# Performance work log

Hardware: AMD Instinct MI355X
Metric: run time of the kernel (lower is better)

Reference implementation:

```python
import jax, jax.numpy as jnp
import numpy as np

B, L, C = 16, 4096, 32
D = 512
W = 24                  # rolling window
LAGS = [3, 5, 7]
MAXLEN = 5000
EPS = 1e-5


def setup_inputs() -> dict:
    key = jax.random.key(0)
    ks = jax.random.split(key, 8)
    return {
        "x": jax.random.normal(ks[0], (B, L, C), jnp.float32),
        "conv_w": jax.random.normal(ks[1], (D, C * (5 + len(LAGS)), 3), jnp.float32) * 0.05,
        "conv_b": jnp.zeros((D,), jnp.float32),
        "learned_pe": jax.random.normal(ks[2], (1, MAXLEN, D), jnp.float32) * (1.0 / np.sqrt(D)),
        "tape_pos": jax.random.normal(ks[3], (MAXLEN, D), jnp.float32) * 0.02,
        "tproj_w": jax.random.normal(ks[4], (D, D), jnp.float32) * 0.02,
        "tproj_b": jnp.zeros((D,), jnp.float32),
        "mixer_w": jax.random.normal(ks[5], (D, 2 * D), jnp.float32) * 0.02,
        "mixer_b": jnp.zeros((D,), jnp.float32),
        "g_c": jnp.ones((D,), jnp.float32), "b_c": jnp.zeros((D,), jnp.float32),
        "g_f": jnp.ones((D,), jnp.float32), "b_f": jnp.zeros((D,), jnp.float32),
        "g_l": jnp.ones((D,), jnp.float32), "b_l": jnp.zeros((D,), jnp.float32),
        "g_t": jnp.ones((D,), jnp.float32), "b_t": jnp.zeros((D,), jnp.float32),
        "weight_params": jnp.array([0.25, 0.25, 0.25, 0.25], jnp.float32),
    }


def _layer_norm(h, g, b):
    m = jnp.mean(h, axis=-1, keepdims=True)
    v = jnp.mean((h - m) ** 2, axis=-1, keepdims=True)
    return g * (h - m) / jnp.sqrt(v + EPS) + b


def reference(x, conv_w, conv_b, learned_pe, tape_pos, tproj_w, tproj_b,
              mixer_w, mixer_b, g_c, b_c, g_f, b_f, g_l, b_l, g_t, b_t,
              weight_params):
    Bx, Lx, Cx = x.shape
    # --- RollingFeatureExtractor: replicate-pad left, sliding mean/max/min/std
    xp = jnp.pad(x, ((0, 0), (W - 1, 0), (0, 0)), mode="edge")          # [B, L+W-1, C]
    win = jnp.stack([xp[:, i:i + Lx, :] for i in range(W)], axis=2)       # [B, L, W, C]
    w_mean = jnp.mean(win, axis=2)
    w_max = jnp.max(win, axis=2)
    w_min = jnp.min(win, axis=2)
    w_var = jnp.sum((win - w_mean[:, :, None, :]) ** 2, axis=2) / (W - 1)  # unbiased, torch.std default
    w_std = jnp.sqrt(w_var)
    x_stats = jnp.concatenate([x, w_mean, w_max, w_min, w_std], axis=-1)  # [B, L, 5C]
    # --- lag differences (replicate pad left by max lag)
    ml = max(LAGS)
    xl = jnp.pad(x, ((0, 0), (ml, 0), (0, 0)), mode="edge")
    x_lags = jnp.concatenate([x - xl[:, ml - l:ml - l + Lx, :] for l in LAGS], axis=-1)  # [B, L, 3C]
    comb = jnp.concatenate([x_stats, x_lags], axis=-1)                    # [B, L, 8C]
    # --- TokenEmbedding: Conv1d k=3, circular padding
    h = comb.transpose(0, 2, 1)                                           # [B, 8C, L]
    h = jnp.pad(h, ((0, 0), (0, 0), (1, 1)), mode="wrap")
    h = jax.lax.conv_general_dilated(h, conv_w, (1,), "VALID",
                                     dimension_numbers=("NCH", "OIH", "NCH"))
    h = h + conv_b[None, :, None]
    combined_emb = _layer_norm(h.transpose(0, 2, 1), g_c, b_c)            # [B, L, D]
    # --- fixed sinusoidal PE (constant / detached)
    pos = jnp.arange(Lx)
    div = jnp.exp(jnp.arange(0, D, 2).astype(x.dtype) * (-(np.log(10000.0) / D)))
    ang = pos[:, None].astype(x.dtype) * div[None, :]                     # [L, D/2]
    pe_fixed_tab = jnp.zeros((Lx, D), x.dtype).at[:, 0::2].set(jnp.sin(ang)).at[:, 1::2].set(jnp.cos(ang))
    pe_fixed = _layer_norm(pe_fixed_tab, g_f, b_f)[None]                  # [1, L, D]
    # --- learnable PE
    pe_learned = _layer_norm(learned_pe[:, :Lx], g_l, b_l)                # [1, L, D]
    # --- tAPE: token proj + learned pos embedding -> mixer linear
    pe = tape_pos[pos]                                                    # [L, D]
    tok = combined_emb @ tproj_w.T + tproj_b                              # [B, L, D]
    mixed = jnp.concatenate([tok, jnp.broadcast_to(pe[None], tok.shape)], axis=-1)
    pe_tape = _layer_norm(mixed @ mixer_w.T + mixer_b, g_t, b_t)          # [B, L, D]
    # --- softmax-weighted sum (dropout is identity in eval)
    w = jax.nn.softmax(weight_params)
    return (w[0] * combined_emb + w[1] * pe_fixed + w[2] * pe_learned + w[3] * pe_tape)
```

## Files before the change

kernel.cpp:

```cpp
#include <hip/hip_runtime.h>
#include <stdint.h>


typedef unsigned short u16;
using short8  = __attribute__((ext_vector_type(8))) short;
using floatx4 = __attribute__((ext_vector_type(4))) float;
typedef __attribute__((address_space(1))) const unsigned int u32_as1;
typedef __attribute__((address_space(3))) unsigned int       u32_as3;

static __device__ __forceinline__ u16 f2b(float f) {
  unsigned u = __float_as_uint(f);
  u += 0x7FFFu + ((u >> 16) & 1u);
  return (u16)(u >> 16);
}
static __device__ __forceinline__ float b2f(u16 h) {
  return __uint_as_float(((unsigned)h) << 16);
}

__global__ __launch_bounds__(256) void prep_mats(
    const float* __restrict__ conv_w, const float* __restrict__ mixer_w,
    const float* __restrict__ tproj_w, const float* __restrict__ tape_pos,
    u16* __restrict__ W1, u16* __restrict__ A_m1, u16* __restrict__ M2t,
    u16* __restrict__ tprojT, u16* __restrict__ tape_bf) {
  int i = blockIdx.x * 256 + threadIdx.x;
  if (i < 393216) {
    int d = i / 768, rem = i - d * 768;
    int j = rem >> 8, c = rem & 255;
    W1[i] = f2b(conv_w[(d * 256 + c) * 3 + j]);
  } else if (i < 393216 + 262144) {
    int k = i - 393216; int p = k >> 9, r = k & 511;
    A_m1[k] = f2b(mixer_w[p * 1024 + r]);
  } else if (i < 393216 + 524288) {
    int k = i - 393216 - 262144; int p = k >> 9, r = k & 511;
    M2t[k] = f2b(mixer_w[p * 1024 + 512 + r]);
  } else if (i < 393216 + 786432) {
    int k = i - 393216 - 524288; int q = k >> 9, r = k & 511;
    tprojT[k] = f2b(tproj_w[r * 512 + q]);
  } else if (i < 393216 + 786432 + 2097152) {
    int k = i - 393216 - 786432;
    tape_bf[k] = f2b(tape_pos[k]);
  }
}

__global__ __launch_bounds__(256) void bias2_k(
    const float* __restrict__ mixer_w, const float* __restrict__ tproj_b,
    const float* __restrict__ mixer_b, float* __restrict__ bias2) {
  int p = blockIdx.x * 256 + threadIdx.x;
  if (p < 512) {
    float s = mixer_b[p];
    for (int r = 0; r < 512; ++r) s += mixer_w[p * 1024 + r] * tproj_b[r];
    bias2[p] = s;
  }
}

__global__ __launch_bounds__(256) void feat_kernel(
    const float* __restrict__ x, u16* __restrict__ comb) {
  __shared__ float sx[87 * 32];
  const int b = blockIdx.y, l0 = blockIdx.x * 64;
  for (int idx = threadIdx.x; idx < 87 * 32; idx += 256) {
    int r = idx >> 5, c = idx & 31;
    int ls = l0 - 23 + r; if (ls < 0) ls = 0;
    sx[idx] = x[((size_t)b * 4096 + ls) * 32 + c];
  }
  __syncthreads();
  const int c = threadIdx.x & 31, lr0 = threadIdx.x >> 5;
  for (int pass = 0; pass < 8; ++pass) {
    int lr = pass * 8 + lr0;
    int l = l0 + lr;
    float w[24];
    float s = 0.f, mx = -3.4e38f, mn = 3.4e38f;
    #pragma unroll
    for (int i = 0; i < 24; ++i) {
      float v = sx[(lr + i) * 32 + c];
      w[i] = v; s += v; mx = fmaxf(mx, v); mn = fminf(mn, v);
    }
    float mean = s * (1.f / 24.f);
    float ssd = 0.f;
    #pragma unroll
    for (int i = 0; i < 24; ++i) { float d = w[i] - mean; ssd += d * d; }
    float sd = sqrtf(fmaxf(ssd, 0.f) * (1.f / 23.f));
    float xv = w[23];
    float lag3 = xv - sx[(lr + 20) * 32 + c];
    float lag5 = xv - sx[(lr + 18) * 32 + c];
    float lag7 = xv - sx[(lr + 16) * 32 + c];
    size_t base = ((size_t)b * 4096 + l) * 256 + c;
    comb[base +   0] = f2b(xv);
    comb[base +  32] = f2b(mean);
    comb[base +  64] = f2b(mx);
    comb[base +  96] = f2b(mn);
    comb[base + 128] = f2b(sd);
    comb[base + 160] = f2b(lag3);
    comb[base + 192] = f2b(lag5);
    comb[base + 224] = f2b(lag7);
  }
}

__global__ __launch_bounds__(256) void gemm_bt(
    const u16* __restrict__ A, const u16* __restrict__ Bt,
    void* __restrict__ outp, int K, int ldc,
    const float* __restrict__ bias, int outBf16) {
  __shared__ __align__(16) u16 lA[128 * 64];
  __shared__ __align__(16) u16 lB[128 * 64];
  const int tid = threadIdx.x;
  const int m0 = blockIdx.x * 128, n0 = blockIdx.y * 128;
  const int wave = tid >> 6, lane = tid & 63;
  const int wm = (wave & 1) * 64, wn = (wave >> 1) * 64;
  const int quad = lane >> 4, r16 = lane & 15;
  const int rowT = tid >> 3, col8 = tid & 7;

  floatx4 acc[4][4];
  #pragma unroll
  for (int i = 0; i < 4; ++i)
    #pragma unroll
    for (int j = 0; j < 4; ++j) acc[i][j] = (floatx4){0.f, 0.f, 0.f, 0.f};

  for (int kk = 0; kk < K; kk += 64) {
    __syncthreads();
    #pragma unroll
    for (int it = 0; it < 4; ++it) {
      int rr = it * 32 + rowT;
      const u16* ga = A  + (size_t)(m0 + rr) * K + kk + col8 * 8;
      const u16* gb = Bt + (size_t)(n0 + rr) * K + kk + col8 * 8;
      __builtin_amdgcn_global_load_lds((u32_as1*)ga, (u32_as3*)&lA[rr * 64 + col8 * 8], 16, 0, 0);
      __builtin_amdgcn_global_load_lds((u32_as1*)gb, (u32_as3*)&lB[rr * 64 + col8 * 8], 16, 0, 0);
    }
    __syncthreads();
    #pragma unroll
    for (int ks = 0; ks < 64; ks += 32) {
      short8 af[4], bfr[4];
      #pragma unroll
      for (int i = 0; i < 4; ++i)
        af[i] = *(const short8*)&lA[(wm + i * 16 + r16) * 64 + ks + quad * 8];
      #pragma unroll
      for (int j = 0; j < 4; ++j)
        bfr[j] = *(const short8*)&lB[(wn + j * 16 + r16) * 64 + ks + quad * 8];
      #pragma unroll
      for (int i = 0; i < 4; ++i)
        #pragma unroll
        for (int j = 0; j < 4; ++j)
          acc[i][j] = __builtin_amdgcn_mfma_f32_16x16x32_bf16(af[i], bfr[j], acc[i][j], 0, 0, 0);
    }
  }
  #pragma unroll
  for (int i = 0; i < 4; ++i) {
    #pragma unroll
    for (int rr = 0; rr < 4; ++rr) {
      int m = m0 + wm + i * 16 + quad * 4 + rr;
      #pragma unroll
      for (int j = 0; j < 4; ++j) {
        int n = n0 + wn + j * 16 + r16;
        float v = acc[i][j][rr];
        if (bias) v += bias[n];
        if (outBf16) ((u16*)outp)[(size_t)m * ldc + n] = f2b(v);
        else         ((float*)outp)[(size_t)m * ldc + n] = v;
      }
    }
  }
}


#define STAGE_A(SRCEXPR)                                                       \
  _Pragma("unroll")                                                            \
  for (int it = 0; it < 2; ++it) {                                             \
    int id = it * 256 + tid, row = id >> 3, c = id & 7;                        \
    int cg = ((c ^ (row & 7)) << 3);                                           \
    const u16* gsrc = (SRCEXPR);                                               \
    __builtin_amdgcn_global_load_lds((u32_as1*)gsrc,                           \
        (u32_as3*)(smem + id * 16), 16, 0, 0);                                 \
  }
#define STAGE_B(SRCEXPR)                                                       \
  _Pragma("unroll")                                                            \
  for (int it = 0; it < 16; ++it) {                                            \
    int id = it * 256 + tid, row = id >> 3, c = id & 7;                        \
    int cg = ((c ^ (row & 7)) << 3);                                           \
    const u16* gsrc = (SRCEXPR);                                               \
    __builtin_amdgcn_global_load_lds((u32_as1*)gsrc,                           \
        (u32_as3*)(smem + 8192 + id * 16), 16, 0, 0);                          \
  }

__global__ __launch_bounds__(256, 2) void gemm_conv_ln(
    const u16* __restrict__ comb, const u16* __restrict__ W1,
    const float* __restrict__ conv_b, const float* __restrict__ g_c,
    const float* __restrict__ b_c, u16* __restrict__ ce) {
  __shared__ __align__(16) char smem[73728];
  __shared__ float sG[512], sB[512], sBias[512];
  u16* lA = (u16*)smem;
  u16* lB = (u16*)(smem + 8192);
  u16* lT = (u16*)smem;

  const int tid = threadIdx.x;
  if (tid < 128) {
    ((float4*)sG)[tid]    = ((const float4*)g_c)[tid];
    ((float4*)sB)[tid]    = ((const float4*)b_c)[tid];
    ((float4*)sBias)[tid] = ((const float4*)conv_b)[tid];
  }
  const int m0 = blockIdx.x * 64;
  const int b = m0 >> 12, l0 = m0 & 4095;
  const int w = tid >> 6, lane = tid & 63;
  const int quad = lane >> 4, r16 = lane & 15;

  floatx4 acc[4][8];
  #pragma unroll
  for (int i = 0; i < 4; ++i)
    #pragma unroll
    for (int jj = 0; jj < 8; ++jj) acc[i][jj] = (floatx4){0.f, 0.f, 0.f, 0.f};

  for (int kk = 0; kk < 768; kk += 64) {
    const int jsh = kk >> 8, kc = kk & 255;
    __syncthreads();
    STAGE_A(comb + (((size_t)b * 4096 + ((l0 + row + jsh - 1 + 4096) & 4095)) << 8) + kc + cg)
    STAGE_B(W1 + (size_t)row * 768 + kk + cg)
    __syncthreads();
    #pragma unroll
    for (int ks = 0; ks < 64; ks += 32) {
      short8 af[4];
      #pragma unroll
      for (int i = 0; i < 4; ++i) {
        int row = i * 16 + r16;
        af[i] = *(const short8*)&lA[row * 64 + ((((ks >> 3) + quad) ^ (row & 7)) << 3)];
      }
      #pragma unroll
      for (int jj = 0; jj < 8; ++jj) {
        int row = w * 128 + jj * 16 + r16;
        short8 bf = *(const short8*)&lB[row * 64 + ((((ks >> 3) + quad) ^ (row & 7)) << 3)];
        #pragma unroll
        for (int i = 0; i < 4; ++i)
          acc[i][jj] = __builtin_amdgcn_mfma_f32_16x16x32_bf16(bf, af[i], acc[i][jj], 0, 0, 0);
      }
    }
  }
  __syncthreads();
  #pragma unroll
  for (int jj = 0; jj < 8; ++jj) {
    int n = w * 128 + jj * 16 + quad * 4;
    float4 b4 = *(const float4*)&sBias[n];
    #pragma unroll
    for (int i = 0; i < 4; ++i) {
      ushort4 pk;
      pk.x = f2b(acc[i][jj][0] + b4.x);
      pk.y = f2b(acc[i][jj][1] + b4.y);
      pk.z = f2b(acc[i][jj][2] + b4.z);
      pk.w = f2b(acc[i][jj][3] + b4.w);
      *(ushort4*)(lT + (size_t)(i * 16 + r16) * 520 + n) = pk;
    }
  }
  __syncthreads();
  const int orow = tid >> 2, part = tid & 3;
  const u16* rowp = lT + (size_t)orow * 520;
  float s1 = 0.f, s2 = 0.f;
  #pragma unroll
  for (int k = 0; k < 16; ++k) {
    short8 t8 = *(const short8*)(rowp + (part + k * 4) * 8);
    #pragma unroll
    for (int e = 0; e < 8; ++e) {
      float f = b2f((u16)t8[e]); s1 += f; s2 += f * f;
    }
  }
  s1 += __shfl_xor(s1, 1); s2 += __shfl_xor(s2, 1);
  s1 += __shfl_xor(s1, 2); s2 += __shfl_xor(s2, 2);
  float mean = s1 * (1.f / 512.f);
  float inv = rsqrtf(fmaxf(s2 * (1.f / 512.f) - mean * mean, 0.f) + 1e-5f);
  size_t mrow = (size_t)(m0 + orow) * 512;
  #pragma unroll
  for (int k = 0; k < 16; ++k) {
    int c8 = part + k * 4;
    short8 t8 = *(const short8*)(rowp + c8 * 8);
    short8 o;
    #pragma unroll
    for (int e = 0; e < 8; ++e) {
      int d = c8 * 8 + e;
      o[e] = (short)f2b(sG[d] * ((b2f((u16)t8[e]) - mean) * inv) + sB[d]);
    }
    *(short8*)(ce + mrow + c8 * 8) = o;
  }
}

__global__ __launch_bounds__(256, 2) void gemm_pre_final(
    const u16* __restrict__ ceA, const u16* __restrict__ Wf,
    const u16* __restrict__ ctab_bf, const u16* __restrict__ pf_tab,
    const u16* __restrict__ pl_tab, const float* __restrict__ g_t,
    const float* __restrict__ b_t, const float* __restrict__ wp,
    float* __restrict__ out) {
  __shared__ __align__(16) char smem[73728];
  __shared__ float sG[512], sB[512];
  u16* lA = (u16*)smem;
  u16* lB = (u16*)(smem + 8192);
  u16* lT = (u16*)smem;

  const int tid = threadIdx.x;
  if (tid < 128) {
    ((float4*)sG)[tid] = ((const float4*)g_t)[tid];
    ((float4*)sB)[tid] = ((const float4*)b_t)[tid];
  }
  const int m0 = blockIdx.x * 64;
  const int l0m = m0 & 4095;
  const int w = tid >> 6, lane = tid & 63;
  const int quad = lane >> 4, r16 = lane & 15;

  floatx4 acc[4][8];
  #pragma unroll
  for (int i = 0; i < 4; ++i)
    #pragma unroll
    for (int jj = 0; jj < 8; ++jj) acc[i][jj] = (floatx4){0.f, 0.f, 0.f, 0.f};

  for (int kk = 0; kk < 512; kk += 64) {
    __syncthreads();
    STAGE_A(ceA + (size_t)(m0 + row) * 512 + kk + cg)
    STAGE_B(Wf + (size_t)row * 512 + kk + cg)
    __syncthreads();
    #pragma unroll
    for (int ks = 0; ks < 64; ks += 32) {
      short8 af[4];
      #pragma unroll
      for (int i = 0; i < 4; ++i) {
        int row = i * 16 + r16;
        af[i] = *(const short8*)&lA[row * 64 + ((((ks >> 3) + quad) ^ (row & 7)) << 3)];
      }
      #pragma unroll
      for (int jj = 0; jj < 8; ++jj) {
        int row = w * 128 + jj * 16 + r16;
        short8 bf = *(const short8*)&lB[row * 64 + ((((ks >> 3) + quad) ^ (row & 7)) << 3)];
        #pragma unroll
        for (int i = 0; i < 4; ++i)
          acc[i][jj] = __builtin_amdgcn_mfma_f32_16x16x32_bf16(bf, af[i], acc[i][jj], 0, 0, 0);
      }
    }
  }
  __syncthreads();
  #pragma unroll
  for (int jj = 0; jj < 8; ++jj) {
    int n = w * 128 + jj * 16 + quad * 4;
    #pragma unroll
    for (int i = 0; i < 4; ++i) {
      ushort4 pk;
      pk.x = f2b(acc[i][jj][0]);
      pk.y = f2b(acc[i][jj][1]);
      pk.z = f2b(acc[i][jj][2]);
      pk.w = f2b(acc[i][jj][3]);
      *(ushort4*)(lT + (size_t)(i * 16 + r16) * 520 + n) = pk;
    }
  }
  __syncthreads();
  const int orow = tid >> 2, part = tid & 3;
  const int m = m0 + orow, l = l0m + orow;
  const u16* rowp = lT + (size_t)orow * 520;
  const size_t lrow = (size_t)l * 512, mrow = (size_t)m * 512;
  float s1 = 0.f, s2 = 0.f;
  #pragma unroll
  for (int k = 0; k < 16; ++k) {
    int c8 = part + k * 4;
    short8 t8 = *(const short8*)(rowp + c8 * 8);
    short8 ct = *(const short8*)(ctab_bf + lrow + c8 * 8);
    #pragma unroll
    for (int e = 0; e < 8; ++e) {
      float f = b2f((u16)t8[e]) + b2f((u16)ct[e]);
      s1 += f; s2 += f * f;
    }
  }
  s1 += __shfl_xor(s1, 1); s2 += __shfl_xor(s2, 1);
  s1 += __shfl_xor(s1, 2); s2 += __shfl_xor(s2, 2);
  float mean = s1 * (1.f / 512.f);
  float inv = rsqrtf(fmaxf(s2 * (1.f / 512.f) - mean * mean, 0.f) + 1e-5f);

  float a0 = wp[0], a1 = wp[1], a2 = wp[2], a3 = wp[3];
  float mxw = fmaxf(fmaxf(a0, a1), fmaxf(a2, a3));
  float e0 = expf(a0 - mxw), e1 = expf(a1 - mxw), e2 = expf(a2 - mxw), e3 = expf(a3 - mxw);
  float invs = 1.f / (e0 + e1 + e2 + e3);
  float w0 = e0 * invs, w1 = e1 * invs, w2 = e2 * invs, w3 = e3 * invs;

  #pragma unroll
  for (int k = 0; k < 16; ++k) {
    int c8 = part + k * 4;
    short8 t8  = *(const short8*)(rowp + c8 * 8);
    short8 ct  = *(const short8*)(ctab_bf + lrow + c8 * 8);
    short8 c8v = *(const short8*)(ceA + mrow + c8 * 8);
    short8 pf  = *(const short8*)(pf_tab + lrow + c8 * 8);
    short8 pl  = *(const short8*)(pl_tab + lrow + c8 * 8);
    float o[8];
    #pragma unroll
    for (int e = 0; e < 8; ++e) {
      int d = c8 * 8 + e;
      float f = b2f((u16)t8[e]) + b2f((u16)ct[e]);
      float pt = sG[d] * ((f - mean) * inv) + sB[d];
      o[e] = w0 * b2f((u16)c8v[e]) + w1 * b2f((u16)pf[e]) + w2 * b2f((u16)pl[e]) + w3 * pt;
    }
    float4* op = (float4*)(out + mrow + c8 * 8);
    op[0] = make_float4(o[0], o[1], o[2], o[3]);
    op[1] = make_float4(o[4], o[5], o[6], o[7]);
  }
}

__global__ __launch_bounds__(256) void pe_tables(
    const float* __restrict__ learned_pe,
    const float* __restrict__ gf, const float* __restrict__ bf_,
    const float* __restrict__ gl, const float* __restrict__ bl,
    u16* __restrict__ pf_tab, u16* __restrict__ pl_tab) {
  int row = blockIdx.x * 4 + (threadIdx.x >> 6);
  int lane = threadIdx.x & 63;
  size_t base = (size_t)row * 512 + lane * 8;
  float v[8]; float s1 = 0.f, s2 = 0.f;
  #pragma unroll
  for (int e = 0; e < 8; ++e) {
    int d = lane * 8 + e;
    int de = d & ~1;
    float div = expf((float)de * (-9.210340371976184f / 512.f));
    float ang = (float)row * div;
    v[e] = (d & 1) ? cosf(ang) : sinf(ang);
    s1 += v[e]; s2 += v[e] * v[e];
  }
  #pragma unroll
  for (int off = 32; off; off >>= 1) { s1 += __shfl_xor(s1, off); s2 += __shfl_xor(s2, off); }
  float mean = s1 * (1.f / 512.f);
  float inv = rsqrtf(fmaxf(s2 * (1.f / 512.f) - mean * mean, 0.f) + 1e-5f);
  short8 o;
  #pragma unroll
  for (int e = 0; e < 8; ++e) {
    int d = lane * 8 + e;
    o[e] = (short)f2b(gf[d] * ((v[e] - mean) * inv) + bf_[d]);
  }
  *(short8*)(pf_tab + base) = o;
  const float4* lp = (const float4*)(learned_pe + base);
  float4 a = lp[0], bq = lp[1];
  float u[8] = {a.x, a.y, a.z, a.w, bq.x, bq.y, bq.z, bq.w};
  s1 = 0.f; s2 = 0.f;
  #pragma unroll
  for (int e = 0; e < 8; ++e) { s1 += u[e]; s2 += u[e] * u[e]; }
  #pragma unroll
  for (int off = 32; off; off >>= 1) { s1 += __shfl_xor(s1, off); s2 += __shfl_xor(s2, off); }
  mean = s1 * (1.f / 512.f);
  inv = rsqrtf(fmaxf(s2 * (1.f / 512.f) - mean * mean, 0.f) + 1e-5f);
  #pragma unroll
  for (int e = 0; e < 8; ++e) {
    int d = lane * 8 + e;
    o[e] = (short)f2b(gl[d] * ((u[e] - mean) * inv) + bl[d]);
  }
  *(short8*)(pl_tab + base) = o;
}

extern "C" void kernel_launch(void* const* d_in, const int* in_sizes, int n_in,
                              void* d_out, int out_size, void* d_ws, size_t ws_size,
                              hipStream_t stream) {
  const float* x          = (const float*)d_in[0];
  const float* conv_w     = (const float*)d_in[1];
  const float* conv_b     = (const float*)d_in[2];
  const float* learned_pe = (const float*)d_in[3];
  const float* tape_pos   = (const float*)d_in[4];
  const float* tproj_w    = (const float*)d_in[5];
  const float* tproj_b    = (const float*)d_in[6];
  const float* mixer_w    = (const float*)d_in[7];
  const float* mixer_b    = (const float*)d_in[8];
  const float* g_c        = (const float*)d_in[9];
  const float* b_c        = (const float*)d_in[10];
  const float* g_f        = (const float*)d_in[11];
  const float* b_f        = (const float*)d_in[12];
  const float* g_l        = (const float*)d_in[13];
  const float* b_l        = (const float*)d_in[14];
  const float* g_t        = (const float*)d_in[15];
  const float* b_t        = (const float*)d_in[16];
  const float* wp         = (const float*)d_in[17];

  char* ws = (char*)d_ws;
  u16*  comb    = (u16*)(ws + 0);
  u16*  ce      = (u16*)(ws + 33554432);
  char* S       = ws + 100663296;
  u16*  W1      = (u16*)(S + 0);
  u16*  A_m1    = (u16*)(S + 786432);
  u16*  M2t     = (u16*)(S + 1310720);
  u16*  tprojT  = (u16*)(S + 1835008);
  u16*  tape_bf = (u16*)(S + 2359296);
  u16*  Wf      = (u16*)(S + 6553600);
  u16*  ctab_bf = (u16*)(S + 7077888);
  float* bias2  = (float*)(S + 11272192);
  u16*  pf_tab  = (u16*)(S + 11274240);
  u16*  pl_tab  = (u16*)(S + 15468544);

  prep_mats<<<12800, 256, 0, stream>>>(conv_w, mixer_w, tproj_w, tape_pos,
                                       W1, A_m1, M2t, tprojT, tape_bf);
  bias2_k<<<2, 256, 0, stream>>>(mixer_w, tproj_b, mixer_b, bias2);
  feat_kernel<<<dim3(64, 16), 256, 0, stream>>>(x, comb);
  gemm_bt<<<dim3(4, 4), 256, 0, stream>>>(A_m1, tprojT, Wf, 512, 512, nullptr, 1);
  gemm_bt<<<dim3(32, 4), 256, 0, stream>>>(tape_bf, M2t, ctab_bf, 512, 512, bias2, 1);
  pe_tables<<<1024, 256, 0, stream>>>(learned_pe, g_f, b_f, g_l, b_l, pf_tab, pl_tab);
  gemm_conv_ln<<<1024, 256, 0, stream>>>(comb, W1, conv_b, g_c, b_c, ce);
  gemm_pre_final<<<1024, 256, 0, stream>>>(ce, Wf, ctab_bf, pf_tab, pl_tab,
                                           g_t, b_t, wp, (float*)d_out);
}
```

Measured before the change: 390.8 us.

## Double GEMM M-tile to 128 rows with 512-thread blocks sharing B tile

Both fused GEMM kernels now process 128 rows per block with 8 waves arranged 2x4, so each staged 512x64 weight tile in LDS serves twice as many output rows. This halves the total weight-tile reloads from L2 and the grid size. The LayerNorm epilogue runs in two 64-row halves through the shared LDS transpose buffer, which adds extra barriers. LDS per block grows to about 88KB, so likely only one block fits per CU, giving the same wave count as before but less freedom in scheduling.

```diff
diff --git a/kernel.cpp b/kernel.cpp
--- a/kernel.cpp
+++ b/kernel.cpp
@@ -162,7 +162,7 @@
 #define STAGE_A(SRCEXPR)                                                       \
   _Pragma("unroll")                                                            \
   for (int it = 0; it < 2; ++it) {                                             \
-    int id = it * 256 + tid, row = id >> 3, c = id & 7;                        \
+    int id = it * 512 + tid, row = id >> 3, c = id & 7;                        \
     int cg = ((c ^ (row & 7)) << 3);                                           \
     const u16* gsrc = (SRCEXPR);                                               \
     __builtin_amdgcn_global_load_lds((u32_as1*)gsrc,                           \
@@ -170,22 +170,22 @@
   }
 #define STAGE_B(SRCEXPR)                                                       \
   _Pragma("unroll")                                                            \
-  for (int it = 0; it < 16; ++it) {                                            \
-    int id = it * 256 + tid, row = id >> 3, c = id & 7;                        \
+  for (int it = 0; it < 8; ++it) {                                             \
+    int id = it * 512 + tid, row = id >> 3, c = id & 7;                        \
     int cg = ((c ^ (row & 7)) << 3);                                           \
     const u16* gsrc = (SRCEXPR);                                               \
     __builtin_amdgcn_global_load_lds((u32_as1*)gsrc,                           \
-        (u32_as3*)(smem + 8192 + id * 16), 16, 0, 0);                          \
-  }
-
-__global__ __launch_bounds__(256, 2) void gemm_conv_ln(
+        (u32_as3*)(smem + 16384 + id * 16), 16, 0, 0);                         \
+  }
+
+__global__ __launch_bounds__(512, 2) void gemm_conv_ln(
     const u16* __restrict__ comb, const u16* __restrict__ W1,
     const float* __restrict__ conv_b, const float* __restrict__ g_c,
     const float* __restrict__ b_c, u16* __restrict__ ce) {
-  __shared__ __align__(16) char smem[73728];
+  __shared__ __align__(16) char smem[81920];
   __shared__ float sG[512], sB[512], sBias[512];
   u16* lA = (u16*)smem;
-  u16* lB = (u16*)(smem + 8192);
+  u16* lB = (u16*)(smem + 16384);
   u16* lT = (u16*)smem;
 
   const int tid = threadIdx.x;
@@ -194,10 +194,11 @@
     ((float4*)sB)[tid]    = ((const float4*)b_c)[tid];
     ((float4*)sBias)[tid] = ((const float4*)conv_b)[tid];
   }
-  const int m0 = blockIdx.x * 64;
+  const int m0 = blockIdx.x * 128;
   const int b = m0 >> 12, l0 = m0 & 4095;
   const int w = tid >> 6, lane = tid & 63;
   const int quad = lane >> 4, r16 = lane & 15;
+  const int wm2 = w >> 2, wn = (w & 3) * 128;
 
   floatx4 acc[4][8];
   #pragma unroll
@@ -216,12 +217,12 @@
       short8 af[4];
       #pragma unroll
       for (int i = 0; i < 4; ++i) {
-        int row = i * 16 + r16;
+        int row = wm2 * 64 + i * 16 + r16;
         af[i] = *(const short8*)&lA[row * 64 + ((((ks >> 3) + quad) ^ (row & 7)) << 3)];
       }
       #pragma unroll
       for (int jj = 0; jj < 8; ++jj) {
-        int row = w * 128 + jj * 16 + r16;
+        int row = wn + jj * 16 + r16;
         short8 bf = *(const short8*)&lB[row * 64 + ((((ks >> 3) + quad) ^ (row & 7)) << 3)];
         #pragma unroll
         for (int i = 0; i < 4; ++i)
@@ -230,61 +231,68 @@
     }
   }
   __syncthreads();
-  #pragma unroll
-  for (int jj = 0; jj < 8; ++jj) {
-    int n = w * 128 + jj * 16 + quad * 4;
-    float4 b4 = *(const float4*)&sBias[n];
-    #pragma unroll
-    for (int i = 0; i < 4; ++i) {
-      ushort4 pk;
-      pk.x = f2b(acc[i][jj][0] + b4.x);
-      pk.y = f2b(acc[i][jj][1] + b4.y);
-      pk.z = f2b(acc[i][jj][2] + b4.z);
-      pk.w = f2b(acc[i][jj][3] + b4.w);
-      *(ushort4*)(lT + (size_t)(i * 16 + r16) * 520 + n) = pk;
-    }
-  }
-  __syncthreads();
-  const int orow = tid >> 2, part = tid & 3;
-  const u16* rowp = lT + (size_t)orow * 520;
-  float s1 = 0.f, s2 = 0.f;
-  #pragma unroll
-  for (int k = 0; k < 16; ++k) {
-    short8 t8 = *(const short8*)(rowp + (part + k * 4) * 8);
-    #pragma unroll
-    for (int e = 0; e < 8; ++e) {
-      float f = b2f((u16)t8[e]); s1 += f; s2 += f * f;
-    }
-  }
-  s1 += __shfl_xor(s1, 1); s2 += __shfl_xor(s2, 1);
-  s1 += __shfl_xor(s1, 2); s2 += __shfl_xor(s2, 2);
-  float mean = s1 * (1.f / 512.f);
-  float inv = rsqrtf(fmaxf(s2 * (1.f / 512.f) - mean * mean, 0.f) + 1e-5f);
-  size_t mrow = (size_t)(m0 + orow) * 512;
-  #pragma unroll
-  for (int k = 0; k < 16; ++k) {
-    int c8 = part + k * 4;
-    short8 t8 = *(const short8*)(rowp + c8 * 8);
-    short8 o;
-    #pragma unroll
-    for (int e = 0; e < 8; ++e) {
-      int d = c8 * 8 + e;
-      o[e] = (short)f2b(sG[d] * ((b2f((u16)t8[e]) - mean) * inv) + sB[d]);
-    }
-    *(short8*)(ce + mrow + c8 * 8) = o;
-  }
-}
-
-__global__ __launch_bounds__(256, 2) void gemm_pre_final(
+  const int orow = tid >> 3, part = tid & 7;
+  #pragma unroll
+  for (int h = 0; h < 2; ++h) {
+    if (wm2 == h) {
+      #pragma unroll
+      for (int jj = 0; jj < 8; ++jj) {
+        int n = wn + jj * 16 + quad * 4;
+        float4 b4 = *(const float4*)&sBias[n];
+        #pragma unroll
+        for (int i = 0; i < 4; ++i) {
+          ushort4 pk;
+          pk.x = f2b(acc[i][jj][0] + b4.x);
+          pk.y = f2b(acc[i][jj][1] + b4.y);
+          pk.z = f2b(acc[i][jj][2] + b4.z);
+          pk.w = f2b(acc[i][jj][3] + b4.w);
+          *(ushort4*)(lT + (size_t)(i * 16 + r16) * 520 + n) = pk;
+        }
+      }
+    }
+    __syncthreads();
+    const u16* rowp = lT + (size_t)orow * 520;
+    float s1 = 0.f, s2 = 0.f;
+    #pragma unroll
+    for (int k = 0; k < 8; ++k) {
+      short8 t8 = *(const short8*)(rowp + (part + k * 8) * 8);
+      #pragma unroll
+      for (int e = 0; e < 8; ++e) {
+        float f = b2f((u16)t8[e]); s1 += f; s2 += f * f;
+      }
+    }
+    s1 += __shfl_xor(s1, 1); s2 += __shfl_xor(s2, 1);
+    s1 += __shfl_xor(s1, 2); s2 += __shfl_xor(s2, 2);
+    s1 += __shfl_xor(s1, 4); s2 += __shfl_xor(s2, 4);
+    float mean = s1 * (1.f / 512.f);
+    float inv = rsqrtf(fmaxf(s2 * (1.f / 512.f) - mean * mean, 0.f) + 1e-5f);
+    size_t mrow = (size_t)(m0 + h * 64 + orow) * 512;
+    #pragma unroll
+    for (int k = 0; k < 8; ++k) {
+      int c8 = part + k * 8;
+      short8 t8 = *(const short8*)(rowp + c8 * 8);
+      short8 o;
+      #pragma unroll
+      for (int e = 0; e < 8; ++e) {
+        int d = c8 * 8 + e;
+        o[e] = (short)f2b(sG[d] * ((b2f((u16)t8[e]) - mean) * inv) + sB[d]);
+      }
+      *(short8*)(ce + mrow + c8 * 8) = o;
+    }
+    __syncthreads();
+  }
+}
+
+__global__ __launch_bounds__(512, 2) void gemm_pre_final(
     const u16* __restrict__ ceA, const u16* __restrict__ Wf,
     const u16* __restrict__ ctab_bf, const u16* __restrict__ pf_tab,
     const u16* __restrict__ pl_tab, const float* __restrict__ g_t,
     const float* __restrict__ b_t, const float* __restrict__ wp,
     float* __restrict__ out) {
-  __shared__ __align__(16) char smem[73728];
+  __shared__ __align__(16) char smem[81920];
   __shared__ float sG[512], sB[512];
   u16* lA = (u16*)smem;
-  u16* lB = (u16*)(smem + 8192);
+  u16* lB = (u16*)(smem + 16384);
   u16* lT = (u16*)smem;
 
   const int tid = threadIdx.x;
@@ -292,10 +300,11 @@
     ((float4*)sG)[tid] = ((const float4*)g_t)[tid];
     ((float4*)sB)[tid] = ((const float4*)b_t)[tid];
   }
-  const int m0 = blockIdx.x * 64;
+  const int m0 = blockIdx.x * 128;
   const int l0m = m0 & 4095;
   const int w = tid >> 6, lane = tid & 63;
   const int quad = lane >> 4, r16 = lane & 15;
+  const int wm2 = w >> 2, wn = (w & 3) * 128;
 
   floatx4 acc[4][8];
   #pragma unroll
@@ -313,12 +322,12 @@
       short8 af[4];
       #pragma unroll
       for (int i = 0; i < 4; ++i) {
-        int row = i * 16 + r16;
+        int row = wm2 * 64 + i * 16 + r16;
         af[i] = *(const short8*)&lA[row * 64 + ((((ks >> 3) + quad) ^ (row & 7)) << 3)];
       }
       #pragma unroll
       for (int jj = 0; jj < 8; ++jj) {
-        int row = w * 128 + jj * 16 + r16;
+        int row = wn + jj * 16 + r16;
         short8 bf = *(const short8*)&lB[row * 64 + ((((ks >> 3) + quad) ^ (row & 7)) << 3)];
         #pragma unroll
         for (int i = 0; i < 4; ++i)
@@ -327,40 +336,7 @@
     }
   }
   __syncthreads();
-  #pragma unroll
-  for (int jj = 0; jj < 8; ++jj) {
-    int n = w * 128 + jj * 16 + quad * 4;
-    #pragma unroll
-    for (int i = 0; i < 4; ++i) {
-      ushort4 pk;
-      pk.x = f2b(acc[i][jj][0]);
-      pk.y = f2b(acc[i][jj][1]);
-      pk.z = f2b(acc[i][jj][2]);
-      pk.w = f2b(acc[i][jj][3]);
-      *(ushort4*)(lT + (size_t)(i * 16 + r16) * 520 + n) = pk;
-    }
-  }
-  __syncthreads();
-  const int orow = tid >> 2, part = tid & 3;
-  const int m = m0 + orow, l = l0m + orow;
-  const u16* rowp = lT + (size_t)orow * 520;
-  const size_t lrow = (size_t)l * 512, mrow = (size_t)m * 512;
-  float s1 = 0.f, s2 = 0.f;
-  #pragma unroll
-  for (int k = 0; k < 16; ++k) {
-    int c8 = part + k * 4;
-    short8 t8 = *(const short8*)(rowp + c8 * 8);
-    short8 ct = *(const short8*)(ctab_bf + lrow + c8 * 8);
-    #pragma unroll
-    for (int e = 0; e < 8; ++e) {
-      float f = b2f((u16)t8[e]) + b2f((u16)ct[e]);
-      s1 += f; s2 += f * f;
-    }
-  }
-  s1 += __shfl_xor(s1, 1); s2 += __shfl_xor(s2, 1);
-  s1 += __shfl_xor(s1, 2); s2 += __shfl_xor(s2, 2);
-  float mean = s1 * (1.f / 512.f);
-  float inv = rsqrtf(fmaxf(s2 * (1.f / 512.f) - mean * mean, 0.f) + 1e-5f);
+  const int orow = tid >> 3, part = tid & 7;
 
   float a0 = wp[0], a1 = wp[1], a2 = wp[2], a3 = wp[3];
   float mxw = fmaxf(fmaxf(a0, a1), fmaxf(a2, a3));
@@ -369,24 +345,65 @@
   float w0 = e0 * invs, w1 = e1 * invs, w2 = e2 * invs, w3 = e3 * invs;
 
   #pragma unroll
-  for (int k = 0; k < 16; ++k) {
-    int c8 = part + k * 4;
-    short8 t8  = *(const short8*)(rowp + c8 * 8);
-    short8 ct  = *(const short8*)(ctab_bf + lrow + c8 * 8);
-    short8 c8v = *(const short8*)(ceA + mrow + c8 * 8);
-    short8 pf  = *(const short8*)(pf_tab + lrow + c8 * 8);
-    short8 pl  = *(const short8*)(pl_tab + lrow + c8 * 8);
-    float o[8];
-    #pragma unroll
-    for (int e = 0; e < 8; ++e) {
-      int d = c8 * 8 + e;
-      float f = b2f((u16)t8[e]) + b2f((u16)ct[e]);
-      float pt = sG[d] * ((f - mean) * inv) + sB[d];
-      o[e] = w0 * b2f((u16)c8v[e]) + w1 * b2f((u16)pf[e]) + w2 * b2f((u16)pl[e]) + w3 * pt;
-    }
-    float4* op = (float4*)(out + mrow + c8 * 8);
-    op[0] = make_float4(o[0], o[1], o[2], o[3]);
-    op[1] = make_float4(o[4], o[5], o[6], o[7]);
+  for (int h = 0; h < 2; ++h) {
+    if (wm2 == h) {
+      #pragma unroll
+      for (int jj = 0; jj < 8; ++jj) {
+        int n = wn + jj * 16 + quad * 4;
+        #pragma unroll
+        for (int i = 0; i < 4; ++i) {
+          ushort4 pk;
+          pk.x = f2b(acc[i][jj][0]);
+          pk.y = f2b(acc[i][jj][1]);
+          pk.z = f2b(acc[i][jj][2]);
+          pk.w = f2b(acc[i][jj][3]);
+          *(ushort4*)(lT + (size_t)(i * 16 + r16) * 520 + n) = pk;
+        }
+      }
+    }
+    __syncthreads();
+    const int m = m0 + h * 64 + orow, l = l0m + h * 64 + orow;
+    const u16* rowp = lT + (size_t)orow * 520;
+    const size_t lrow = (size_t)l * 512, mrow = (size_t)m * 512;
+    float s1 = 0.f, s2 = 0.f;
+    #pragma unroll
+    for (int k = 0; k < 8; ++k) {
+      int c8 = part + k * 8;
+      short8 t8 = *(const short8*)(rowp + c8 * 8);
+      short8 ct = *(const short8*)(ctab_bf + lrow + c8 * 8);
+      #pragma unroll
+      for (int e = 0; e < 8; ++e) {
+        float f = b2f((u16)t8[e]) + b2f((u16)ct[e]);
+        s1 += f; s2 += f * f;
+      }
+    }
+    s1 += __shfl_xor(s1, 1); s2 += __shfl_xor(s2, 1);
+    s1 += __shfl_xor(s1, 2); s2 += __shfl_xor(s2, 2);
+    s1 += __shfl_xor(s1, 4); s2 += __shfl_xor(s2, 4);
+    float mean = s1 * (1.f / 512.f);
+    float inv = rsqrtf(fmaxf(s2 * (1.f / 512.f) - mean * mean, 0.f) + 1e-5f);
+
+    #pragma unroll
+    for (int k = 0; k < 8; ++k) {
+      int c8 = part + k * 8;
+      short8 t8  = *(const short8*)(rowp + c8 * 8);
+      short8 ct  = *(const short8*)(ctab_bf + lrow + c8 * 8);
+      short8 c8v = *(const short8*)(ceA + mrow + c8 * 8);
+      short8 pf  = *(const short8*)(pf_tab + lrow + c8 * 8);
+      short8 pl  = *(const short8*)(pl_tab + lrow + c8 * 8);
+      float o[8];
+      #pragma unroll
+      for (int e = 0; e < 8; ++e) {
+        int d = c8 * 8 + e;
+        float f = b2f((u16)t8[e]) + b2f((u16)ct[e]);
+        float pt = sG[d] * ((f - mean) * inv) + sB[d];
+        o[e] = w0 * b2f((u16)c8v[e]) + w1 * b2f((u16)pf[e]) + w2 * b2f((u16)pl[e]) + w3 * pt;
+      }
+      float4* op = (float4*)(out + mrow + c8 * 8);
+      op[0] = make_float4(o[0], o[1], o[2], o[3]);
+      op[1] = make_float4(o[4], o[5], o[6], o[7]);
+    }
+    __syncthreads();
   }
 }
 
@@ -481,7 +498,7 @@
   gemm_bt<<<dim3(4, 4), 256, 0, stream>>>(A_m1, tprojT, Wf, 512, 512, nullptr, 1);
   gemm_bt<<<dim3(32, 4), 256, 0, stream>>>(tape_bf, M2t, ctab_bf, 512, 512, bias2, 1);
   pe_tables<<<1024, 256, 0, stream>>>(learned_pe, g_f, b_f, g_l, b_l, pf_tab, pl_tab);
-  gemm_conv_ln<<<1024, 256, 0, stream>>>(comb, W1, conv_b, g_c, b_c, ce);
-  gemm_pre_final<<<1024, 256, 0, stream>>>(ce, Wf, ctab_bf, pf_tab, pl_tab,
-                                           g_t, b_t, wp, (float*)d_out);
-}
+  gemm_conv_ln<<<512, 512, 0, stream>>>(comb, W1, conv_b, g_c, b_c, ce);
+  gemm_pre_final<<<512, 512, 0, stream>>>(ce, Wf, ctab_bf, pf_tab, pl_tab,
+                                          g_t, b_t, wp, (float*)d_out);
+}
```

Measured after the change: 414.0 us. 1.06x slower.

## Double-buffer LDS staging in both GEMM kernels with smaller K chunks

Applied to the files above, without the earlier changes.

Both MFMA GEMM kernels now load the next K-slice into a second LDS buffer while computing on the current one, halving the K step from 64 to 32 and switching to a 4-way XOR swizzle. The goal is to hide global-to-LDS load latency and drop one barrier per iteration. In exchange the loop runs twice as many iterations, and correctness relies on the async global_load_lds writes being complete by the single trailing barrier, with no explicit vmcnt wait.

```diff
diff --git a/kernel.cpp b/kernel.cpp
--- a/kernel.cpp
+++ b/kernel.cpp
@@ -159,23 +159,23 @@
 }
 
 
-#define STAGE_A(SRCEXPR)                                                       \
-  _Pragma("unroll")                                                            \
-  for (int it = 0; it < 2; ++it) {                                             \
-    int id = it * 256 + tid, row = id >> 3, c = id & 7;                        \
-    int cg = ((c ^ (row & 7)) << 3);                                           \
-    const u16* gsrc = (SRCEXPR);                                               \
-    __builtin_amdgcn_global_load_lds((u32_as1*)gsrc,                           \
-        (u32_as3*)(smem + id * 16), 16, 0, 0);                                 \
-  }
-#define STAGE_B(SRCEXPR)                                                       \
-  _Pragma("unroll")                                                            \
-  for (int it = 0; it < 16; ++it) {                                            \
-    int id = it * 256 + tid, row = id >> 3, c = id & 7;                        \
-    int cg = ((c ^ (row & 7)) << 3);                                           \
-    const u16* gsrc = (SRCEXPR);                                               \
-    __builtin_amdgcn_global_load_lds((u32_as1*)gsrc,                           \
-        (u32_as3*)(smem + 8192 + id * 16), 16, 0, 0);                          \
+#define STAGE_PAIR(BUFOFF, ASRCEXPR, BSRCEXPR)                                 \
+  {                                                                            \
+    {                                                                          \
+      int id = tid, row = id >> 2, c = id & 3;                                 \
+      int cg = ((c ^ (row & 3)) << 3); (void)cg;                               \
+      const u16* gsrc = (ASRCEXPR);                                            \
+      __builtin_amdgcn_global_load_lds((u32_as1*)gsrc,                         \
+          (u32_as3*)(smem + (BUFOFF) + id * 16), 16, 0, 0);                    \
+    }                                                                          \
+    _Pragma("unroll")                                                          \
+    for (int it = 0; it < 8; ++it) {                                           \
+      int id = it * 256 + tid, row = id >> 2, c = id & 3;                      \
+      int cg = ((c ^ (row & 3)) << 3); (void)cg;                               \
+      const u16* gsrc = (BSRCEXPR);                                            \
+      __builtin_amdgcn_global_load_lds((u32_as1*)gsrc,                         \
+          (u32_as3*)(smem + (BUFOFF) + 4096 + id * 16), 16, 0, 0);             \
+    }                                                                          \
   }
 
 __global__ __launch_bounds__(256, 2) void gemm_conv_ln(
@@ -184,8 +184,6 @@
     const float* __restrict__ b_c, u16* __restrict__ ce) {
   __shared__ __align__(16) char smem[73728];
   __shared__ float sG[512], sB[512], sBias[512];
-  u16* lA = (u16*)smem;
-  u16* lB = (u16*)(smem + 8192);
   u16* lT = (u16*)smem;
 
   const int tid = threadIdx.x;
@@ -198,6 +196,7 @@
   const int b = m0 >> 12, l0 = m0 & 4095;
   const int w = tid >> 6, lane = tid & 63;
   const int quad = lane >> 4, r16 = lane & 15;
+  const int wn = w * 128;
 
   floatx4 acc[4][8];
   #pragma unroll
@@ -205,34 +204,42 @@
     #pragma unroll
     for (int jj = 0; jj < 8; ++jj) acc[i][jj] = (floatx4){0.f, 0.f, 0.f, 0.f};
 
-  for (int kk = 0; kk < 768; kk += 64) {
-    const int jsh = kk >> 8, kc = kk & 255;
+  STAGE_PAIR(0,
+      comb + (((size_t)b * 4096 + ((l0 + row - 1 + 4096) & 4095)) << 8) + cg,
+      W1 + (size_t)row * 768 + cg)
+  __syncthreads();
+
+  for (int t = 0; t < 24; ++t) {
+    const int cur = t & 1;
+    const u16* lAc = (const u16*)(smem + cur * 36864);
+    const u16* lBc = (const u16*)(smem + cur * 36864 + 4096);
+    if (t + 1 < 24) {
+      const int skk = (t + 1) * 32;
+      const int sj = skk >> 8, skc = skk & 255;
+      STAGE_PAIR((1 - cur) * 36864,
+          comb + (((size_t)b * 4096 + ((l0 + row + sj - 1 + 4096) & 4095)) << 8) + skc + cg,
+          W1 + (size_t)row * 768 + skk + cg)
+    }
+    short8 af[4];
+    #pragma unroll
+    for (int i = 0; i < 4; ++i) {
+      int row = i * 16 + r16;
+      af[i] = *(const short8*)&lAc[row * 32 + ((quad ^ (row & 3)) << 3)];
+    }
+    #pragma unroll
+    for (int jj = 0; jj < 8; ++jj) {
+      int row = wn + jj * 16 + r16;
+      short8 bf = *(const short8*)&lBc[row * 32 + ((quad ^ (row & 3)) << 3)];
+      #pragma unroll
+      for (int i = 0; i < 4; ++i)
+        acc[i][jj] = __builtin_amdgcn_mfma_f32_16x16x32_bf16(bf, af[i], acc[i][jj], 0, 0, 0);
+    }
     __syncthreads();
-    STAGE_A(comb + (((size_t)b * 4096 + ((l0 + row + jsh - 1 + 4096) & 4095)) << 8) + kc + cg)
-    STAGE_B(W1 + (size_t)row * 768 + kk + cg)
-    __syncthreads();
-    #pragma unroll
-    for (int ks = 0; ks < 64; ks += 32) {
-      short8 af[4];
-      #pragma unroll
-      for (int i = 0; i < 4; ++i) {
-        int row = i * 16 + r16;
-        af[i] = *(const short8*)&lA[row * 64 + ((((ks >> 3) + quad) ^ (row & 7)) << 3)];
-      }
-      #pragma unroll
-      for (int jj = 0; jj < 8; ++jj) {
-        int row = w * 128 + jj * 16 + r16;
-        short8 bf = *(const short8*)&lB[row * 64 + ((((ks >> 3) + quad) ^ (row & 7)) << 3)];
-        #pragma unroll
-        for (int i = 0; i < 4; ++i)
-          acc[i][jj] = __builtin_amdgcn_mfma_f32_16x16x32_bf16(bf, af[i], acc[i][jj], 0, 0, 0);
-      }
-    }
-  }
-  __syncthreads();
+  }
+
   #pragma unroll
   for (int jj = 0; jj < 8; ++jj) {
-    int n = w * 128 + jj * 16 + quad * 4;
+    int n = wn + jj * 16 + quad * 4;
     float4 b4 = *(const float4*)&sBias[n];
     #pragma unroll
     for (int i = 0; i < 4; ++i) {
@@ -283,8 +290,6 @@
     float* __restrict__ out) {
   __shared__ __align__(16) char smem[73728];
   __shared__ float sG[512], sB[512];
-  u16* lA = (u16*)smem;
-  u16* lB = (u16*)(smem + 8192);
   u16* lT = (u16*)smem;
 
   const int tid = threadIdx.x;
@@ -296,6 +301,7 @@
   const int l0m = m0 & 4095;
   const int w = tid >> 6, lane = tid & 63;
   const int quad = lane >> 4, r16 = lane & 15;
+  const int wn = w * 128;
 
   floatx4 acc[4][8];
   #pragma unroll
@@ -303,33 +309,41 @@
     #pragma unroll
     for (int jj = 0; jj < 8; ++jj) acc[i][jj] = (floatx4){0.f, 0.f, 0.f, 0.f};
 
-  for (int kk = 0; kk < 512; kk += 64) {
+  STAGE_PAIR(0,
+      ceA + (size_t)(m0 + row) * 512 + cg,
+      Wf + (size_t)row * 512 + cg)
+  __syncthreads();
+
+  for (int t = 0; t < 16; ++t) {
+    const int cur = t & 1;
+    const u16* lAc = (const u16*)(smem + cur * 36864);
+    const u16* lBc = (const u16*)(smem + cur * 36864 + 4096);
+    if (t + 1 < 16) {
+      const int skk = (t + 1) * 32;
+      STAGE_PAIR((1 - cur) * 36864,
+          ceA + (size_t)(m0 + row) * 512 + skk + cg,
+          Wf + (size_t)row * 512 + skk + cg)
+    }
+    short8 af[4];
+    #pragma unroll
+    for (int i = 0; i < 4; ++i) {
+      int row = i * 16 + r16;
+      af[i] = *(const short8*)&lAc[row * 32 + ((quad ^ (row & 3)) << 3)];
+    }
+    #pragma unroll
+    for (int jj = 0; jj < 8; ++jj) {
+      int row = wn + jj * 16 + r16;
+      short8 bf = *(const short8*)&lBc[row * 32 + ((quad ^ (row & 3)) << 3)];
+      #pragma unroll
+      for (int i = 0; i < 4; ++i)
+        acc[i][jj] = __builtin_amdgcn_mfma_f32_16x16x32_bf16(bf, af[i], acc[i][jj], 0, 0, 0);
+    }
     __syncthreads();
-    STAGE_A(ceA + (size_t)(m0 + row) * 512 + kk + cg)
-    STAGE_B(Wf + (size_t)row * 512 + kk + cg)
-    __syncthreads();
-    #pragma unroll
-    for (int ks = 0; ks < 64; ks += 32) {
-      short8 af[4];
-      #pragma unroll
-      for (int i = 0; i < 4; ++i) {
-        int row = i * 16 + r16;
-        af[i] = *(const short8*)&lA[row * 64 + ((((ks >> 3) + quad) ^ (row & 7)) << 3)];
-      }
-      #pragma unroll
-      for (int jj = 0; jj < 8; ++jj) {
-        int row = w * 128 + jj * 16 + r16;
-        short8 bf = *(const short8*)&lB[row * 64 + ((((ks >> 3) + quad) ^ (row & 7)) << 3)];
-        #pragma unroll
-        for (int i = 0; i < 4; ++i)
-          acc[i][jj] = __builtin_amdgcn_mfma_f32_16x16x32_bf16(bf, af[i], acc[i][jj], 0, 0, 0);
-      }
-    }
-  }
-  __syncthreads();
+  }
+
   #pragma unroll
   for (int jj = 0; jj < 8; ++jj) {
-    int n = w * 128 + jj * 16 + quad * 4;
+    int n = wn + jj * 16 + quad * 4;
     #pragma unroll
     for (int i = 0; i < 4; ++i) {
       ushort4 pk;
```

Measured after the change: 414.8 us. 6.1% more time.
